# Kernel tuning notes

Hardware: AMD Instinct MI355X
Metric: run time of the kernel (lower is better)

## Reference

```python
import jax, jax.numpy as jnp
import numpy as np

NEG_SLOPE = 0.2  # PyG GATConv default leaky_relu slope


def gat_conv(x, edge_index, W, a_src, a_dst, b):
    """PyG GATConv (heads=1, concat=True, add_self_loops=True, dropout=0)."""
    N = x.shape[0]
    loops = jnp.arange(N, dtype=edge_index.dtype)
    src = jnp.concatenate([edge_index[0], loops])  # [Ef]
    dst = jnp.concatenate([edge_index[1], loops])  # [Ef]
    h = x @ W  # [N, Dout]
    alpha_src = h @ a_src  # [N]
    alpha_dst = h @ a_dst  # [N]
    logits = jax.nn.leaky_relu(alpha_src[src] + alpha_dst[dst], NEG_SLOPE)  # [Ef]
    # segment softmax over edges grouped by destination node
    m = jax.ops.segment_max(logits, dst, num_segments=N)
    e = jnp.exp(logits - m[dst])
    denom = jax.ops.segment_sum(e, dst, num_segments=N)  # >0: every node has a self-loop
    alpha = e / denom[dst]  # [Ef]
    out = jax.ops.segment_sum(alpha[:, None] * h[src], dst, num_segments=N)
    return out + b


def global_mean_pool(x, batch, num_graphs):
    s = jax.ops.segment_sum(x, batch, num_segments=num_graphs)
    cnt = jax.ops.segment_sum(jnp.ones((x.shape[0],), x.dtype), batch, num_segments=num_graphs)
    return s / jnp.maximum(cnt, 1.0)[:, None]


NUM_GRAPHS = 64


def setup_inputs() -> dict:
    key = jax.random.key(0)
    ks = jax.random.split(key, 12)
    N, E, D = 50000, 600000, 128
    x = jax.random.normal(ks[0], (N, D), dtype=jnp.float32)
    edge_index = jax.random.randint(ks[1], (2, E), 0, N, dtype=jnp.int32)
    edge_weight = jax.random.uniform(ks[2], (E,), dtype=jnp.float32)
    batch = jnp.sort(jax.random.randint(ks[3], (N,), 0, NUM_GRAPHS, dtype=jnp.int32))
    sc = 1.0 / np.sqrt(D)
    W0 = jax.random.normal(ks[4], (D, D), dtype=jnp.float32) * sc
    a_src0 = jax.random.normal(ks[5], (D,), dtype=jnp.float32) * sc
    a_dst0 = jax.random.normal(ks[6], (D,), dtype=jnp.float32) * sc
    b0 = jnp.zeros((D,), dtype=jnp.float32)
    W1 = jax.random.normal(ks[7], (D, D), dtype=jnp.float32) * sc
    a_src1 = jax.random.normal(ks[8], (D,), dtype=jnp.float32) * sc
    a_dst1 = jax.random.normal(ks[9], (D,), dtype=jnp.float32) * sc
    b1 = jnp.zeros((D,), dtype=jnp.float32)
    return {"x": x, "edge_index": edge_index, "edge_weight": edge_weight, "batch": batch,
            "W0": W0, "a_src0": a_src0, "a_dst0": a_dst0, "b0": b0,
            "W1": W1, "a_src1": a_src1, "a_dst1": a_dst1, "b1": b1}


def reference(x, edge_index, edge_weight, batch, W0, a_src0, a_dst0, b0, W1, a_src1, a_dst1, b1):
    # layer 0 (relu_layers_index=[0] -> ReLU after layer 0)
    out = gat_conv(x, edge_index, W0, a_src0, a_dst0, b0)
    out = jax.nn.relu(out)
    emb0 = global_mean_pool(out, batch, NUM_GRAPHS)
    # layer 1 (no relu, no dropout)
    out = gat_conv(out, edge_index, W1, a_src1, a_dst1, b1)
    emb1 = global_mean_pool(out, batch, NUM_GRAPHS)
    return (emb0, emb1)
```

## Files before the change

kernel.cpp:

```cpp
#include <hip/hip_runtime.h>

typedef unsigned int u32;
typedef unsigned short u16;
typedef unsigned long long u64;

typedef short bf16x8 __attribute__((ext_vector_type(8)));
typedef float f32x4 __attribute__((ext_vector_type(4)));
typedef float f32x2 __attribute__((ext_vector_type(2)));

__device__ __forceinline__ float bl(u32 u){ return __uint_as_float(u << 16); }
__device__ __forceinline__ float bh(u32 u){ return __uint_as_float(u & 0xffff0000u); }
__device__ __forceinline__ float b16f(u16 r){ return __uint_as_float(((u32)r) << 16); }
__device__ __forceinline__ u16 f2b(float f){
  u32 u = __float_as_uint(f);
  u32 r = (u + 0x7fffu + ((u >> 16) & 1u)) >> 16;
  return (u16)r;
}
__device__ __forceinline__ u32 pk2(float a, float b){
  return (u32)f2b(a) | ((u32)f2b(b) << 16);
}
__device__ __forceinline__ void fma8(float* acc, float e2, uint2 h){
  f32x2 p0 = __builtin_amdgcn_cvt_pk_f32_fp8((int)h.x, 0);
  f32x2 p1 = __builtin_amdgcn_cvt_pk_f32_fp8((int)h.x, 1);
  f32x2 p2 = __builtin_amdgcn_cvt_pk_f32_fp8((int)h.y, 0);
  f32x2 p3 = __builtin_amdgcn_cvt_pk_f32_fp8((int)h.y, 1);
  acc[0]=fmaf(e2,p0.x,acc[0]); acc[1]=fmaf(e2,p0.y,acc[1]);
  acc[2]=fmaf(e2,p1.x,acc[2]); acc[3]=fmaf(e2,p1.y,acc[3]);
  acc[4]=fmaf(e2,p2.x,acc[4]); acc[5]=fmaf(e2,p2.y,acc[5]);
  acc[6]=fmaf(e2,p3.x,acc[6]); acc[7]=fmaf(e2,p3.y,acc[7]);
}

#define NEG_SLOPE 0.2f
#define BSTRIDE 4096


__device__ __forceinline__ int block_detect(const u32* __restrict__ x){
  __shared__ int cnt_;
  if (threadIdx.x == 0) cnt_ = 0;
  __syncthreads();
  u32 w = x[threadIdx.x];
  int e = (int)((w >> 7) & 0xFFu);
  if (e >= 110 && e <= 135) atomicAdd(&cnt_, 1);
  __syncthreads();
  return (cnt_ >= 128) ? 1 : 0;
}

__global__ __launch_bounds__(256) void part_k(const int* __restrict__ ei, int E, int nbuck,
    int* __restrict__ gcnt, u64* __restrict__ breg)
{
  __shared__ u32 hist[256];
  __shared__ u32 lscan[257];
  __shared__ u32 gbase[256];
  __shared__ u32 cur[256];
  __shared__ u64 stage[2048];
  const int tid = threadIdx.x;
  hist[tid] = 0; cur[tid] = 0;
  __syncthreads();
  const int e0 = blockIdx.x * 2048;
  int src[8], dst[8];
  #pragma unroll
  for (int j = 0; j < 8; j++){
    int t = e0 + tid + j*256;
    if (t < E){
      src[j] = ei[t]; dst[j] = ei[E + t];
      atomicAdd(&hist[dst[j] >> 8], 1u);
    } else dst[j] = -1;
  }
  __syncthreads();
  const u32 v = hist[tid];
  lscan[tid] = v;
  __syncthreads();
  for (int off = 1; off < 256; off <<= 1){
    u32 add = (tid >= off) ? lscan[tid - off] : 0;
    __syncthreads();
    lscan[tid] += add;
    __syncthreads();
  }
  if (tid == 255) lscan[256] = lscan[255];
  u32 excl = lscan[tid] - v;
  __syncthreads();
  const u32 total = lscan[256];
  lscan[tid] = excl;
  if (tid < nbuck && v > 0) gbase[tid] = (u32)atomicAdd(&gcnt[tid], (int)v);
  __syncthreads();
  #pragma unroll
  for (int j = 0; j < 8; j++){
    if (dst[j] >= 0){
      int b = dst[j] >> 8;
      u32 p = lscan[b] + atomicAdd(&cur[b], 1u);
      stage[p] = ((u64)(u32)dst[j] << 32) | (u32)src[j];
    }
  }
  __syncthreads();
  for (u32 i = tid; i < total; i += 256){
    u64 e = stage[i];
    int b = (int)(e >> 40);
    u32 r = i - lscan[b];
    breg[(long)b * BSTRIDE + gbase[b] + r] = e;
  }
}

__global__ __launch_bounds__(256) void csr_k(const int* __restrict__ gcnt,
    const u64* __restrict__ breg,
    int* __restrict__ deg, int* __restrict__ rowptr, int* __restrict__ csrc, int N)
{
  __shared__ u32 dl[256];
  __shared__ u32 rp[256];
  __shared__ u32 cu[256];
  const int b = blockIdx.x, tid = threadIdx.x;
  const int n0 = b << 8;
  const int cntb = gcnt[b];
  dl[tid] = 0; cu[tid] = 0;
  __syncthreads();
  const u64* reg = breg + (long)b * BSTRIDE;
  for (int i = tid; i < cntb; i += 256)
    atomicAdd(&dl[(int)(reg[i] >> 32) - n0], 1u);
  __syncthreads();
  const u32 v = dl[tid];
  rp[tid] = v;
  __syncthreads();
  for (int off = 1; off < 256; off <<= 1){
    u32 add = (tid >= off) ? rp[tid - off] : 0;
    __syncthreads();
    rp[tid] += add;
    __syncthreads();
  }
  u32 excl = rp[tid] - v;
  __syncthreads();
  rp[tid] = excl;
  __syncthreads();
  int node = n0 + tid;
  if (node < N){ deg[node] = (int)v; rowptr[node] = b*BSTRIDE + (int)excl; }
  for (int i = tid; i < cntb; i += 256){
    u64 e = reg[i];
    int d = (int)(e >> 32) - n0;
    u32 pos = rp[d] + atomicAdd(&cu[d], 1u);
    csrc[(long)b*BSTRIDE + pos] = (int)(e & 0xffffffffULL);
  }
}

template<bool XEXT, bool KPERM>
__device__ __forceinline__ void gemm_body(int gb, int isbf,
    const void* __restrict__ Xv, const void* __restrict__ Wv,
    const void* __restrict__ av, const void* __restrict__ dv,
    u32* __restrict__ Hb, float* __restrict__ As, float* __restrict__ Ad, int N)
{
  __shared__ u16 Wt[128*136];
  const int tid = threadIdx.x;

  if (isbf){
    const u32* Wp = (const u32*)Wv;
    #pragma unroll
    for (int i = 0; i < 16; i++){
      int idx = tid + i*256;
      u32 p = Wp[idx];
      int k = idx >> 6, n2 = idx & 63;
      int pos = KPERM ? ((k & 15)*8 + (k >> 4)) : k;
      Wt[(2*n2)*136 + pos]   = (u16)(p & 0xffffu);
      Wt[(2*n2+1)*136 + pos] = (u16)(p >> 16);
    }
  } else {
    const float* Wf = (const float*)Wv;
    #pragma unroll
    for (int i = 0; i < 64; i++){
      int idx = tid + i*256;
      int k = idx >> 7, n = idx & 127;
      int pos = KPERM ? ((k & 15)*8 + (k >> 4)) : k;
      Wt[n*136 + pos] = f2b(Wf[idx]);
    }
  }
  __syncthreads();

  const int wv = tid >> 6, L = tid & 63;
  const int row0 = (gb*4 + wv) * 16;
  if (row0 >= N) return;
  const int nl = L & 15, quad = L >> 4;

  bf16x8 af[4];
  if (!XEXT || isbf){
    const uint4* Xr = (const uint4*)(((const u32*)Xv) + (long)row0*64);
    #pragma unroll
    for (int kb = 0; kb < 4; kb++)
      af[kb] = *(const bf16x8*)&Xr[nl*16 + kb*4 + quad];
  } else {
    const float* Xf = ((const float*)Xv) + (long)(row0 + nl)*128;
    #pragma unroll
    for (int kb = 0; kb < 4; kb++){
      const float4* p = (const float4*)(Xf + kb*32 + quad*8);
      float4 f0 = p[0], f1 = p[1];
      uint4 tmp = make_uint4(pk2(f0.x,f0.y), pk2(f0.z,f0.w), pk2(f1.x,f1.y), pk2(f1.z,f1.w));
      af[kb] = *(const bf16x8*)&tmp;
    }
  }

  f32x4 acc[8];
  #pragma unroll
  for (int nt = 0; nt < 8; nt++) acc[nt] = (f32x4){0.f,0.f,0.f,0.f};
  #pragma unroll
  for (int nt = 0; nt < 8; nt++){
    #pragma unroll
    for (int kb = 0; kb < 4; kb++){
      bf16x8 bf = *(const bf16x8*)&Wt[(nt*16 + nl)*136 + kb*32 + quad*8];
      acc[nt] = __builtin_amdgcn_mfma_f32_16x16x32_bf16(af[kb], bf, acc[nt], 0, 0, 0);
    }
  }

  float ps[4] = {0.f,0.f,0.f,0.f}, pd[4] = {0.f,0.f,0.f,0.f};
  #pragma unroll
  for (int nt = 0; nt < 8; nt++){
    int col = nt*16 + nl;
    float a_ = isbf ? b16f(((const u16*)av)[col]) : ((const float*)av)[col];
    float d_ = isbf ? b16f(((const u16*)dv)[col]) : ((const float*)dv)[col];
    #pragma unroll
    for (int r = 0; r < 4; r++){
      ps[r] = fmaf(acc[nt][r], a_, ps[r]);
      pd[r] = fmaf(acc[nt][r], d_, pd[r]);
    }
  }
  #pragma unroll
  for (int off = 1; off < 16; off <<= 1){
    #pragma unroll
    for (int r = 0; r < 4; r++){
      ps[r] += __shfl_xor(ps[r], off);
      pd[r] += __shfl_xor(pd[r], off);
    }
  }
  if (nl == 0){
    #pragma unroll
    for (int r = 0; r < 4; r++){
      As[row0 + quad*4 + r] = ps[r];
      Ad[row0 + quad*4 + r] = pd[r];
    }
  }

  #pragma unroll
  for (int r = 0; r < 4; r++){
    long row = row0 + quad*4 + r;
    int w0 = 0, w1 = 0;
    w0 = __builtin_amdgcn_cvt_pk_fp8_f32(acc[0][r], acc[1][r], w0, 0);
    w0 = __builtin_amdgcn_cvt_pk_fp8_f32(acc[2][r], acc[3][r], w0, 1);
    w1 = __builtin_amdgcn_cvt_pk_fp8_f32(acc[4][r], acc[5][r], w1, 0);
    w1 = __builtin_amdgcn_cvt_pk_fp8_f32(acc[6][r], acc[7][r], w1, 1);
    uint2 v = make_uint2((u32)w0, (u32)w1);
    *(uint2*)(Hb + row*32 + nl*2) = v;
  }
}

__device__ __forceinline__ void pool_body(const u32* __restrict__ Ob,
    const int* __restrict__ batch, float* __restrict__ psum, int N)
{
  const int tid = threadIdx.x;
  const int wv = tid >> 6, lane = tid & 63;
  const int start = blockIdx.x * 128;
  const int end = min(start + 128, N);
  float2 acc = make_float2(0.f, 0.f);
  int cur = -1;
  for (int node = start + wv; node < end; node += 4){
    int gid = batch[node];
    if (gid != cur){
      if (cur >= 0){
        atomicAdd(&psum[cur*128 + lane*2],     acc.x);
        atomicAdd(&psum[cur*128 + lane*2 + 1], acc.y);
      }
      cur = gid; acc = make_float2(0.f, 0.f);
    }
    u32 p = Ob[(long)node*64 + lane];
    acc.x += bl(p); acc.y += bh(p);
  }
  if (cur >= 0){
    atomicAdd(&psum[cur*128 + lane*2],     acc.x);
    atomicAdd(&psum[cur*128 + lane*2 + 1], acc.y);
  }
}

__global__ __launch_bounds__(256) void gemmdet0_k(
    const u32* __restrict__ x, int* __restrict__ flag,
    const void* __restrict__ W0, const void* __restrict__ as0, const void* __restrict__ ad0,
    u32* __restrict__ Hb, float* __restrict__ As, float* __restrict__ Ad, int N)
{
  int isbf = block_detect(x);
  if (blockIdx.x == 0 && threadIdx.x == 0) *flag = isbf;
  gemm_body<true, false>(blockIdx.x, isbf, x, W0, as0, ad0, Hb, As, Ad, N);
}

__global__ __launch_bounds__(256) void poolgemm1_k(
    const u32* __restrict__ Ob, const int* __restrict__ batch, float* __restrict__ ps0, int pB,
    const void* __restrict__ W1, const void* __restrict__ as1, const void* __restrict__ ad1,
    const int* __restrict__ flag,
    u32* __restrict__ Hb, float* __restrict__ As, float* __restrict__ Ad, int N)
{
  if ((int)blockIdx.x < pB){
    pool_body(Ob, batch, ps0, N);
    return;
  }
  gemm_body<false, true>(blockIdx.x - pB, *flag, Ob, W1, as1, ad1, Hb, As, Ad, N);
}

template<bool RELU>
__global__ __launch_bounds__(256) void gath_k(const int* __restrict__ deg,
    const int* __restrict__ rowptr, const int* __restrict__ csrc,
    const float* __restrict__ As, const float* __restrict__ Ad,
    const u32* __restrict__ Hb, const void* __restrict__ bv, const int* __restrict__ flag,
    u32* __restrict__ Ob, int N)
{
  long t = (long)blockIdx.x*256 + threadIdx.x;
  int node = (int)(t >> 4), q = (int)(t & 15);
  if (node >= N) return;
  const int base = threadIdx.x & 48;
  const float ad = Ad[node];
  float l = As[node] + ad;
  l = l > 0.f ? l : NEG_SLOPE * l;
  float e = __expf(l);
  float acc[8];
  {
    uint2 hv = ((const uint2*)(Hb + (long)node*32))[q];
    f32x2 p0 = __builtin_amdgcn_cvt_pk_f32_fp8((int)hv.x, 0);
    f32x2 p1 = __builtin_amdgcn_cvt_pk_f32_fp8((int)hv.x, 1);
    f32x2 p2 = __builtin_amdgcn_cvt_pk_f32_fp8((int)hv.y, 0);
    f32x2 p3 = __builtin_amdgcn_cvt_pk_f32_fp8((int)hv.y, 1);
    acc[0]=e*p0.x; acc[1]=e*p0.y; acc[2]=e*p1.x; acc[3]=e*p1.y;
    acc[4]=e*p2.x; acc[5]=e*p2.y; acc[6]=e*p3.x; acc[7]=e*p3.y;
  }
  float den = e;
  const int dg = deg[node];
  const int* row = csrc + rowptr[node];
  for (int jb = 0; jb < dg; jb += 16){
    int m = dg - jb; if (m > 16) m = 16;
    int sj = node; float evq = 0.f;
    if (q < m){
      sj = row[jb + q];
      float l2 = As[sj] + ad;
      l2 = l2 > 0.f ? l2 : NEG_SLOPE * l2;
      evq = __expf(l2);
    }
    for (int i = 0; i < m; i += 4){
      float e0 = __shfl(evq, base + i);
      float e1 = __shfl(evq, base + i + 1);
      float e2 = __shfl(evq, base + i + 2);
      float e3 = __shfl(evq, base + i + 3);
      int   s0 = __shfl(sj,  base + i);
      int   s1 = __shfl(sj,  base + i + 1);
      int   s2 = __shfl(sj,  base + i + 2);
      int   s3 = __shfl(sj,  base + i + 3);
      uint2 h0 = ((const uint2*)(Hb + (long)s0*32))[q];
      uint2 h1 = ((const uint2*)(Hb + (long)s1*32))[q];
      uint2 h2 = ((const uint2*)(Hb + (long)s2*32))[q];
      uint2 h3 = ((const uint2*)(Hb + (long)s3*32))[q];
      den += (e0 + e1) + (e2 + e3);
      fma8(acc, e0, h0);
      fma8(acc, e1, h1);
      fma8(acc, e2, h2);
      fma8(acc, e3, h3);
    }
  }
  float inv = 1.f / den;
  float b[8];
  if (*flag){
    const u16* bp = (const u16*)bv;
    #pragma unroll
    for (int i = 0; i < 8; i++) b[i] = b16f(bp[i*16 + q]);
  } else {
    const float* bp = (const float*)bv;
    #pragma unroll
    for (int i = 0; i < 8; i++) b[i] = bp[i*16 + q];
  }
  float o[8];
  #pragma unroll
  for (int i = 0; i < 8; i++){
    o[i] = fmaf(acc[i], inv, b[i]);
    if (RELU) o[i] = fmaxf(o[i], 0.f);
  }
  uint4 w = make_uint4(pk2(o[0],o[1]), pk2(o[2],o[3]), pk2(o[4],o[5]), pk2(o[6],o[7]));
  *(uint4*)&Ob[(long)node*64 + q*4] = w;
}

__global__ __launch_bounds__(256) void pool2_k(const u32* __restrict__ Ob,
    const int* __restrict__ batch, float* __restrict__ psum, int N)
{
  pool_body(Ob, batch, psum, N);
}

__global__ __launch_bounds__(256) void fin_k(const float* __restrict__ ps0,
    const float* __restrict__ ps1, const int* __restrict__ batch, int N,
    const int* __restrict__ flag, void* __restrict__ out)
{
  int t = blockIdx.x*256 + threadIdx.x;
  if (t >= 8192) return;
  int g = t >> 7, pos = t & 127;
  int c = ((pos & 7) << 4) + (pos >> 3);
  int lo = 0, hi = N;
  while (lo < hi){ int mid = (lo + hi) >> 1; if (batch[mid] < g) lo = mid + 1; else hi = mid; }
  int a = lo;
  lo = 0; hi = N;
  while (lo < hi){ int mid = (lo + hi) >> 1; if (batch[mid] < g + 1) lo = mid + 1; else hi = mid; }
  int cc = lo - a;
  float cf = (float)(cc < 1 ? 1 : cc);
  float v0 = ps0[t] / cf, v1 = ps1[t] / cf;
  if (*flag){
    u16* o = (u16*)out;
    o[g*128 + c] = f2b(v0); o[8192 + g*128 + c] = f2b(v1);
  } else {
    float* o = (float*)out;
    o[g*128 + c] = v0; o[8192 + g*128 + c] = v1;
  }
}

extern "C" void kernel_launch(void* const* d_in, const int* in_sizes, int n_in,
                              void* d_out, int out_size, void* d_ws, size_t ws_size,
                              hipStream_t stream)
{
  const void* x    = d_in[0];
  const int* ei    = (const int*)d_in[1];
  const int* batch = (const int*)d_in[3];
  const void* W0  = d_in[4];
  const void* as0 = d_in[5];
  const void* ad0 = d_in[6];
  const void* b0  = d_in[7];
  const void* W1  = d_in[8];
  const void* as1 = d_in[9];
  const void* ad1 = d_in[10];
  const void* b1  = d_in[11];

  const int N  = in_sizes[0] / 128;
  const int E  = in_sizes[1] / 2;
  const int nbuck = (N + 255) >> 8;

  char* ws = (char*)d_ws;
  size_t off = 0;
  auto al = [&](size_t bytes){ size_t o = off; off += (bytes + 255) & ~(size_t)255; return o; };
  u32*   Hb    = (u32*)(ws + al((size_t)N*32*4));
  u32*   Ob    = (u32*)(ws + al((size_t)N*64*4));
  float* As    = (float*)(ws + al((size_t)N*4));
  float* Ad    = (float*)(ws + al((size_t)N*4));
  u64*   breg  = (u64*)(ws + al((size_t)nbuck*BSTRIDE*8));
  int*   csrc  = (int*)(ws + al((size_t)nbuck*BSTRIDE*4));
  int*   deg   = (int*)(ws + al((size_t)N*4));
  int*   rowptr= (int*)(ws + al((size_t)N*4));
  char*  z0    = ws + al(2*64*128*4 + 256*4);
  float* ps0   = (float*)z0;
  float* ps1   = ps0 + 8192;
  int*   gcnt  = (int*)(ps1 + 8192);
  int*   flag  = (int*)(ws + al(256));
  if (off > ws_size) return;

  hipMemsetAsync(z0, 0, 2*64*128*4 + 256*4, stream);

  const int gB   = (N/16 + 3) / 4;
  const int aB   = (E + 2047) / 2048;
  const int nvB16= (N*16 + 255) / 256;
  const int pB   = (N + 127) / 128;

  gemmdet0_k<<<gB, 256, 0, stream>>>((const u32*)x, flag, W0, as0, ad0, Hb, As, Ad, N);
  part_k<<<aB, 256, 0, stream>>>(ei, E, nbuck, gcnt, breg);
  csr_k<<<nbuck, 256, 0, stream>>>(gcnt, breg, deg, rowptr, csrc, N);

  gath_k<true><<<nvB16, 256, 0, stream>>>(deg, rowptr, csrc, As, Ad, Hb, b0, flag, Ob, N);

  poolgemm1_k<<<pB + gB, 256, 0, stream>>>(Ob, batch, ps0, pB,
      W1, as1, ad1, flag, Hb, As, Ad, N);
  gath_k<false><<<nvB16, 256, 0, stream>>>(deg, rowptr, csrc, As, Ad, Hb, b1, flag, Ob, N);
  pool2_k<<<pB, 256, 0, stream>>>(Ob, batch, ps1, N);

  fin_k<<<32, 256, 0, stream>>>(ps0, ps1, batch, N, flag, d_out);
}
```

Baseline: 199.1 us.

## Batch 16 neighbor gathers per step and fuse final pooling into last-block epilogue

The gather inner loop now issues all 16 neighbor row loads up front, with padded lanes pointing at the node itself, instead of 4 at a time. This raises memory-level parallelism at the cost of more registers and some wasted loads on short chunks. Separately, the final normalization kernel is merged into the second pooling kernel. A completion counter elects the last block, which computes the graph boundaries once and writes the outputs, removing one launch and the per-thread binary searches.

```diff
diff --git a/kernel.cpp b/kernel.cpp
--- a/kernel.cpp
+++ b/kernel.cpp
@@ -333,25 +333,21 @@
       l2 = l2 > 0.f ? l2 : NEG_SLOPE * l2;
       evq = __expf(l2);
     }
-    for (int i = 0; i < m; i += 4){
-      float e0 = __shfl(evq, base + i);
-      float e1 = __shfl(evq, base + i + 1);
-      float e2 = __shfl(evq, base + i + 2);
-      float e3 = __shfl(evq, base + i + 3);
-      int   s0 = __shfl(sj,  base + i);
-      int   s1 = __shfl(sj,  base + i + 1);
-      int   s2 = __shfl(sj,  base + i + 2);
-      int   s3 = __shfl(sj,  base + i + 3);
-      uint2 h0 = ((const uint2*)(Hb + (long)s0*32))[q];
-      uint2 h1 = ((const uint2*)(Hb + (long)s1*32))[q];
-      uint2 h2 = ((const uint2*)(Hb + (long)s2*32))[q];
-      uint2 h3 = ((const uint2*)(Hb + (long)s3*32))[q];
-      den += (e0 + e1) + (e2 + e3);
-      fma8(acc, e0, h0);
-      fma8(acc, e1, h1);
-      fma8(acc, e2, h2);
-      fma8(acc, e3, h3);
-    }
+    int s[16];
+    #pragma unroll
+    for (int i = 0; i < 16; i++) s[i] = __shfl(sj, base + i);
+    uint2 h[16];
+    #pragma unroll
+    for (int i = 0; i < 16; i++) h[i] = ((const uint2*)(Hb + (long)s[i]*32))[q];
+    float ev[16];
+    #pragma unroll
+    for (int i = 0; i < 16; i++) ev[i] = __shfl(evq, base + i);
+    float dsum = 0.f;
+    #pragma unroll
+    for (int i = 0; i < 16; i++) dsum += ev[i];
+    den += dsum;
+    #pragma unroll
+    for (int i = 0; i < 16; i++) fma8(acc, ev[i], h[i]);
   }
   float inv = 1.f / den;
   float b[8];
@@ -374,34 +370,42 @@
   *(uint4*)&Ob[(long)node*64 + q*4] = w;
 }
 
-__global__ __launch_bounds__(256) void pool2_k(const u32* __restrict__ Ob,
-    const int* __restrict__ batch, float* __restrict__ psum, int N)
+__global__ __launch_bounds__(256) void pool2fin_k(const u32* __restrict__ Ob,
+    const int* __restrict__ batch, float* __restrict__ psum, int N,
+    int* __restrict__ done, const float* __restrict__ ps0,
+    const int* __restrict__ flag, void* __restrict__ out)
 {
   pool_body(Ob, batch, psum, N);
-}
-
-__global__ __launch_bounds__(256) void fin_k(const float* __restrict__ ps0,
-    const float* __restrict__ ps1, const int* __restrict__ batch, int N,
-    const int* __restrict__ flag, void* __restrict__ out)
-{
-  int t = blockIdx.x*256 + threadIdx.x;
-  if (t >= 8192) return;
-  int g = t >> 7, pos = t & 127;
-  int c = ((pos & 7) << 4) + (pos >> 3);
-  int lo = 0, hi = N;
-  while (lo < hi){ int mid = (lo + hi) >> 1; if (batch[mid] < g) lo = mid + 1; else hi = mid; }
-  int a = lo;
-  lo = 0; hi = N;
-  while (lo < hi){ int mid = (lo + hi) >> 1; if (batch[mid] < g + 1) lo = mid + 1; else hi = mid; }
-  int cc = lo - a;
-  float cf = (float)(cc < 1 ? 1 : cc);
-  float v0 = ps0[t] / cf, v1 = ps1[t] / cf;
-  if (*flag){
-    u16* o = (u16*)out;
-    o[g*128 + c] = f2b(v0); o[8192 + g*128 + c] = f2b(v1);
-  } else {
-    float* o = (float*)out;
-    o[g*128 + c] = v0; o[8192 + g*128 + c] = v1;
+
+  __threadfence();
+  __shared__ int lastF;
+  const int tid = threadIdx.x;
+  if (tid == 0) lastF = (atomicAdd(done, 1) == (int)gridDim.x - 1) ? 1 : 0;
+  __syncthreads();
+  if (!lastF) return;
+
+  __shared__ int bnd[65];
+  if (tid <= 64){
+    int g = tid, lo = 0, hi = N;
+    while (lo < hi){ int mid = (lo + hi) >> 1; if (batch[mid] < g) lo = mid + 1; else hi = mid; }
+    bnd[tid] = lo;
+  }
+  __syncthreads();
+  const int isbf = *flag;
+  for (int t2 = tid; t2 < 8192; t2 += 256){
+    int g = t2 >> 7, pos = t2 & 127;
+    int c = ((pos & 7) << 4) + (pos >> 3);
+    int cc = bnd[g+1] - bnd[g];
+    float cf = (float)(cc < 1 ? 1 : cc);
+    float v0 = ps0[t2] / cf;
+    float v1 = atomicAdd(&psum[t2], 0.f) / cf;
+    if (isbf){
+      u16* op = (u16*)out;
+      op[g*128 + c] = f2b(v0); op[8192 + g*128 + c] = f2b(v1);
+    } else {
+      float* op = (float*)out;
+      op[g*128 + c] = v0; op[8192 + g*128 + c] = v1;
+    }
   }
 }
 
@@ -436,14 +440,16 @@
   int*   csrc  = (int*)(ws + al((size_t)nbuck*BSTRIDE*4));
   int*   deg   = (int*)(ws + al((size_t)N*4));
   int*   rowptr= (int*)(ws + al((size_t)N*4));
-  char*  z0    = ws + al(2*64*128*4 + 256*4);
+  const size_t zbytes = 2*64*128*4 + 256*4 + 256;
+  char*  z0    = ws + al(zbytes);
   float* ps0   = (float*)z0;
   float* ps1   = ps0 + 8192;
   int*   gcnt  = (int*)(ps1 + 8192);
+  int*   done  = (int*)(z0 + 2*64*128*4 + 256*4);
   int*   flag  = (int*)(ws + al(256));
   if (off > ws_size) return;
 
-  hipMemsetAsync(z0, 0, 2*64*128*4 + 256*4, stream);
+  hipMemsetAsync(z0, 0, zbytes, stream);
 
   const int gB   = (N/16 + 3) / 4;
   const int aB   = (E + 2047) / 2048;
@@ -459,7 +465,5 @@
   poolgemm1_k<<<pB + gB, 256, 0, stream>>>(Ob, batch, ps0, pB,
       W1, as1, ad1, flag, Hb, As, Ad, N);
   gath_k<false><<<nvB16, 256, 0, stream>>>(deg, rowptr, csrc, As, Ad, Hb, b1, flag, Ob, N);
-  pool2_k<<<pB, 256, 0, stream>>>(Ob, batch, ps1, N);
-
-  fin_k<<<32, 256, 0, stream>>>(ps0, ps1, batch, N, flag, d_out);
-}
+  pool2fin_k<<<pB, 256, 0, stream>>>(Ob, batch, ps1, N, done, ps0, flag, d_out);
+}
```

Measured after the change: 233.9 us. 1.18x slower.
